# Optimization experiments

Hardware: AMD Instinct MI355X
Metric: run time of the kernel (lower is better)

Reference implementation:

```python
import jax, jax.numpy as jnp
import numpy as np

KEEP_RATIO = 0.5
B, H, W = 8, 1024, 1024


def setup_inputs() -> dict:
    key = jax.random.key(0)
    k1, k2, k3 = jax.random.split(key, 3)
    logits = jax.random.normal(k1, (B, 1, H, W), dtype=jnp.float32)
    targets = jax.random.randint(k2, (B, 1, H, W), 0, 2, dtype=jnp.int32)
    tissue_mask = jax.random.randint(k3, (B, 1, H, W), 0, 2, dtype=jnp.int32)
    return {"logits": logits, "targets": targets, "tissue_mask": tissue_mask}


def reference(logits, targets, tissue_mask):
    b = logits.shape[0]
    x = logits.reshape(b, -1)                       # (B, N)
    t = targets.reshape(b, -1).astype(x.dtype)      # {0,1}
    m = tissue_mask.reshape(b, -1).astype(x.dtype)  # {0,1}
    n = x.shape[1]

    # stable binary_cross_entropy_with_logits, reduction='none'
    bce = jnp.maximum(x, 0.0) - x * t + jnp.log1p(jnp.exp(-jnp.abs(x)))
    loss = bce * m                                  # masked per-pixel loss

    pos = t * m                                     # positives inside tissue
    neg = (1.0 - t) * m                             # negatives inside tissue
    n_pos = jnp.sum(pos, axis=1)                    # (B,)
    n_neg = jnp.sum(neg, axis=1)

    k_all = max(1, int(n * KEEP_RATIO))             # static python int
    # kept count per row: all positives + top-(k_all - n_pos) negatives (clamped)
    k_keep = n_pos + jnp.minimum(jnp.maximum(k_all - n_pos, 0.0), n_neg)  # (B,)

    BIG = jnp.asarray(1e30, x.dtype)
    # sort key: positives always first, then negatives by loss, then non-tissue
    sort_key = jnp.where(pos > 0, BIG, jnp.where(neg > 0, loss, -BIG))
    order = jnp.argsort(-sort_key, axis=1)          # descending
    sorted_loss = jnp.take_along_axis(loss, order, axis=1)

    ranks = jnp.arange(n, dtype=x.dtype)
    keep = (ranks[None, :] < k_keep[:, None]).astype(x.dtype)
    per_sample = jnp.sum(sorted_loss * keep, axis=1) / jnp.maximum(k_keep, 1.0)
    # fallback when no tissue pixels at all: torch keeps index 0 (loss there is 0)
    per_sample = jnp.where(k_keep > 0, per_sample, loss[:, 0])
    return jnp.mean(per_sample)
```

## Files before the change

kernel.cpp:

```cpp
#include <hip/hip_runtime.h>
#include <cstdint>
#include <cstddef>

#define N_PIX   1048576
#define B_ROWS  8
#define K_ALL   524288
#define WG_PER_ROW 256
#define ITERS   4
#define NBINS   2048
#define FPSCALE 262144.0f


__global__ __launch_bounds__(256, 6) void k_pass1(
    const float4* __restrict__ lg, const int4* __restrict__ tg, const int4* __restrict__ mk,
    unsigned long long* __restrict__ hist,
    unsigned* __restrict__ partNpos, double* __restrict__ partSpos, float* __restrict__ out)
{
    __shared__ unsigned long long hq[NBINS];
    __shared__ unsigned swp[4];
    __shared__ double   sws[4];
    const int tid = threadIdx.x;
    for (int b = tid; b < NBINS; b += 256) hq[b] = 0ull;
    if (blockIdx.x == 0 && tid == 0) *out = 0.f;

    const int r = blockIdx.x >> 8;
    const size_t base = (size_t)blockIdx.x * (ITERS * 256) + tid;

    float4 x[ITERS]; int4 t[ITERS]; int4 m[ITERS];
    #pragma unroll
    for (int i = 0; i < ITERS; ++i) {
        x[i] = lg[base + (size_t)i * 256];
        t[i] = tg[base + (size_t)i * 256];
        m[i] = mk[base + (size_t)i * 256];
    }
    __syncthreads();

    unsigned npos = 0; float spos = 0.f;

    auto proc = [&](float xx, int tt, int mm) {
        float ax = fabsf(xx);
        float e = __expf(-ax);
        float l = __logf(1.f + e);
        float bce = fmaxf(xx, 0.f) - xx * (float)tt + l;
        if (mm) {
            if (tt) { npos++; spos += bce; }
            else {
                unsigned bin = __float_as_uint(bce) >> 21;
                if (bin >= NBINS) bin = NBINS - 1;
                unsigned fx = (unsigned)__float2uint_rn(bce * FPSCALE);
                atomicAdd(&hq[bin], (1ull << 48) | (unsigned long long)fx);
            }
        }
    };

    #pragma unroll
    for (int i = 0; i < ITERS; ++i) {
        proc(x[i].x, t[i].x, m[i].x);
        proc(x[i].y, t[i].y, m[i].y);
        proc(x[i].z, t[i].z, m[i].z);
        proc(x[i].w, t[i].w, m[i].w);
    }

    for (int o = 32; o; o >>= 1) {
        npos += __shfl_down(npos, o);
        spos += __shfl_down(spos, o);
    }
    if ((tid & 63) == 0) { swp[tid >> 6] = npos; sws[tid >> 6] = (double)spos; }
    __syncthreads();
    if (tid == 0) {
        partNpos[blockIdx.x] = swp[0] + swp[1] + swp[2] + swp[3];
        partSpos[blockIdx.x] = sws[0] + sws[1] + sws[2] + sws[3];
    }

    unsigned long long* gh = hist + (size_t)r * NBINS;
    for (int b = tid; b < NBINS; b += 256) {
        unsigned long long v = hq[b];
        if (v) atomicAdd(&gh[b], v);
    }
}

__global__ __launch_bounds__(256) void k_final(
    const unsigned long long* __restrict__ hist,
    const unsigned* __restrict__ partNpos, const double* __restrict__ partSpos,
    float* __restrict__ out)
{
    __shared__ unsigned sc[2][256];
    __shared__ double   sd[2][256];
    __shared__ unsigned swp[4];
    __shared__ double   sws[4];
    __shared__ int rT; __shared__ unsigned rcntgt; __shared__ double rsumgt;

    const int r = blockIdx.x, tid = threadIdx.x;
    const unsigned long long* gh = hist + (size_t)r * NBINS;
    const double inv = 1.0 / (double)FPSCALE;

    {
        unsigned np = partNpos[r * 256 + tid];
        double   sp = partSpos[r * 256 + tid];
        for (int o = 32; o; o >>= 1) { np += __shfl_down(np, o); sp += __shfl_down(sp, o); }
        if ((tid & 63) == 0) { swp[tid >> 6] = np; sws[tid >> 6] = sp; }
    }
    __syncthreads();
    const unsigned npos = swp[0] + swp[1] + swp[2] + swp[3];
    const double sumPos = sws[0] + sws[1] + sws[2] + sws[3];
    __syncthreads();

    const int per = NBINS / 256;
    const int b0 = NBINS - 1 - tid * per;
    unsigned lc[8]; double lsum[8];
    unsigned pc = 0; double ps = 0.0;
    #pragma unroll
    for (int i = 0; i < per; ++i) {
        unsigned long long v = gh[b0 - i];
        lc[i] = (unsigned)(v >> 48);
        lsum[i] = (double)(v & 0xFFFFFFFFFFFFull) * inv;
        pc += lc[i]; ps += lsum[i];
    }

    int pp = 0;
    sc[0][tid] = pc; sd[0][tid] = ps;
    __syncthreads();
    for (int ofs = 1; ofs < 256; ofs <<= 1) {
        unsigned c = sc[pp][tid]; double s = sd[pp][tid];
        if (tid >= ofs) { c += sc[pp][tid - ofs]; s += sd[pp][tid - ofs]; }
        sc[pp ^ 1][tid] = c; sd[pp ^ 1][tid] = s;
        pp ^= 1;
        __syncthreads();
    }
    const unsigned nneg   = sc[pp][255];
    const double   sumNeg = sd[pp][255];

    long kl = (long)K_ALL - (long)npos;
    if (kl < 0) kl = 0;
    if (kl > (long)nneg) kl = (long)nneg;
    const unsigned Kneg = (unsigned)kl;

    double sum_sel = 0.0;
    if (Kneg >= nneg) {
        sum_sel = sumNeg;
    } else if (Kneg > 0) {
        unsigned inc = sc[pp][tid];
        unsigned exc = inc - pc;
        double   exs = sd[pp][tid] - ps;
        if (exc < Kneg && Kneg <= inc) {
            unsigned cum = exc; double csum = exs;
            #pragma unroll
            for (int i = 0; i < per; ++i) {
                if (cum + lc[i] >= Kneg) { rT = b0 - i; rcntgt = cum; rsumgt = csum; break; }
                cum += lc[i]; csum += lsum[i];
            }
        }
        __syncthreads();
        if (tid == 0) {
            const int T1 = rT;
            unsigned long long v = gh[T1];
            const unsigned cntT1 = (unsigned)(v >> 48);
            const double   sumT1 = (double)(v & 0xFFFFFFFFFFFFull) * inv;
            const unsigned Kp = Kneg - rcntgt;
            const float lo = __uint_as_float((unsigned)T1 << 21);
            const float hi = __uint_as_float((unsigned)(T1 + 1) << 21);
            const double w = (double)hi - (double)lo;
            const double avg = sumT1 / (double)cntT1;
            const double topmean = avg + 0.5 * w * (1.0 - (double)Kp / (double)cntT1);
            sum_sel = rsumgt + (double)Kp * topmean;
        }
    }

    if (tid == 0) {
        unsigned long long kk = (unsigned long long)npos + (unsigned long long)Kneg;
        double per_s = 0.0;
        if (kk > 0) per_s = (sumPos + sum_sel) / (double)kk;
        atomicAdd(out, (float)(per_s / (double)B_ROWS));
    }
}

extern "C" void kernel_launch(void* const* d_in, const int* in_sizes, int n_in,
                              void* d_out, int out_size, void* d_ws, size_t ws_size,
                              hipStream_t stream)
{
    const float* logits = (const float*)d_in[0];
    const int*   targets = (const int*)d_in[1];
    const int*   tissue = (const int*)d_in[2];

    const int NBLK = B_ROWS * WG_PER_ROW;
    char* ws = (char*)d_ws;
    size_t off = 0;
    unsigned long long* hist = (unsigned long long*)(ws + off);
    off += (size_t)B_ROWS * NBINS * 8;
    size_t zero_size = off;
    unsigned* partNpos = (unsigned*)(ws + off); off += (size_t)NBLK * 4;
    double*   partSpos = (double*)(ws + off);   off += (size_t)NBLK * 8;

    hipMemsetAsync(ws, 0, zero_size, stream);

    k_pass1<<<NBLK, 256, 0, stream>>>(
        (const float4*)logits, (const int4*)targets, (const int4*)tissue,
        hist, partNpos, partSpos, (float*)d_out);
    k_final<<<B_ROWS, 256, 0, stream>>>(hist, partNpos, partSpos, (float*)d_out);
}
```

Baseline: 121.5 us.

## Select top-k negatives via complement: histogram only low-loss negatives below pivot

Instead of histogramming every negative's loss to find the top-K, the kernel now accumulates the total count and sum of negatives and histograms only those below a pivot of 0.25, using 512 bins instead of 2048. The final kernel subtracts the sum of the smallest D = nneg - Kneg negatives, so fewer shared-memory atomics and a smaller global histogram are needed. Loads are split into two chunks to cut register pressure, and occupancy is raised to 8. It assumes the dropped bottom D negatives usually fall under the pivot; otherwise it approximates them at the pivot value, which is an accuracy risk.

After: 121.6 us. No clear change (+0.1%).

```diff
diff --git a/kernel.cpp b/kernel.cpp
--- a/kernel.cpp
+++ b/kernel.cpp
@@ -7,73 +7,84 @@
 #define K_ALL   524288
 #define WG_PER_ROW 256
 #define ITERS   4
-#define NBINS   2048
-#define FPSCALE 262144.0f
-
-
-__global__ __launch_bounds__(256, 6) void k_pass1(
+#define HBINS   512
+#define PIVOT   0.25f
+#define FPSCALE 1048576.0f
+#define MASK48  0xFFFFFFFFFFFFull
+
+
+__global__ __launch_bounds__(256, 8) void k_pass1(
     const float4* __restrict__ lg, const int4* __restrict__ tg, const int4* __restrict__ mk,
     unsigned long long* __restrict__ hist,
-    unsigned* __restrict__ partNpos, double* __restrict__ partSpos, float* __restrict__ out)
+    unsigned* __restrict__ partNpos, unsigned* __restrict__ partNneg,
+    double* __restrict__ partSpos, double* __restrict__ partSneg, float* __restrict__ out)
 {
-    __shared__ unsigned long long hq[NBINS];
-    __shared__ unsigned swp[4];
-    __shared__ double   sws[4];
+    __shared__ unsigned long long hq[HBINS];
+    __shared__ unsigned swp[4], swn[4];
+    __shared__ double   sws[4], swn2[4];
     const int tid = threadIdx.x;
-    for (int b = tid; b < NBINS; b += 256) hq[b] = 0ull;
+    for (int b = tid; b < HBINS; b += 256) hq[b] = 0ull;
     if (blockIdx.x == 0 && tid == 0) *out = 0.f;
+    __syncthreads();
 
     const int r = blockIdx.x >> 8;
     const size_t base = (size_t)blockIdx.x * (ITERS * 256) + tid;
 
-    float4 x[ITERS]; int4 t[ITERS]; int4 m[ITERS];
-    #pragma unroll
-    for (int i = 0; i < ITERS; ++i) {
-        x[i] = lg[base + (size_t)i * 256];
-        t[i] = tg[base + (size_t)i * 256];
-        m[i] = mk[base + (size_t)i * 256];
-    }
-    __syncthreads();
-
-    unsigned npos = 0; float spos = 0.f;
+    unsigned npos = 0, nneg = 0; float spos = 0.f, sneg = 0.f;
 
     auto proc = [&](float xx, int tt, int mm) {
         float ax = fabsf(xx);
-        float e = __expf(-ax);
-        float l = __logf(1.f + e);
+        float l = __logf(1.f + __expf(-ax));
         float bce = fmaxf(xx, 0.f) - xx * (float)tt + l;
         if (mm) {
             if (tt) { npos++; spos += bce; }
             else {
-                unsigned bin = __float_as_uint(bce) >> 21;
-                if (bin >= NBINS) bin = NBINS - 1;
-                unsigned fx = (unsigned)__float2uint_rn(bce * FPSCALE);
-                atomicAdd(&hq[bin], (1ull << 48) | (unsigned long long)fx);
+                nneg++; sneg += bce;
+                if (bce < PIVOT) {
+                    unsigned bin = __float_as_uint(bce) >> 21;
+                    unsigned long long fx = (unsigned long long)__float2uint_rn(bce * FPSCALE);
+                    atomicAdd(&hq[bin], (1ull << 48) | fx);
+                }
             }
         }
     };
 
     #pragma unroll
-    for (int i = 0; i < ITERS; ++i) {
-        proc(x[i].x, t[i].x, m[i].x);
-        proc(x[i].y, t[i].y, m[i].y);
-        proc(x[i].z, t[i].z, m[i].z);
-        proc(x[i].w, t[i].w, m[i].w);
+    for (int c = 0; c < 2; ++c) {
+        float4 x0 = lg[base + (size_t)(2 * c) * 256];
+        float4 x1 = lg[base + (size_t)(2 * c + 1) * 256];
+        int4   t0 = tg[base + (size_t)(2 * c) * 256];
+        int4   t1 = tg[base + (size_t)(2 * c + 1) * 256];
+        int4   m0 = mk[base + (size_t)(2 * c) * 256];
+        int4   m1 = mk[base + (size_t)(2 * c + 1) * 256];
+        proc(x0.x, t0.x, m0.x); proc(x0.y, t0.y, m0.y);
+        proc(x0.z, t0.z, m0.z); proc(x0.w, t0.w, m0.w);
+        proc(x1.x, t1.x, m1.x); proc(x1.y, t1.y, m1.y);
+        proc(x1.z, t1.z, m1.z); proc(x1.w, t1.w, m1.w);
     }
 
     for (int o = 32; o; o >>= 1) {
         npos += __shfl_down(npos, o);
+        nneg += __shfl_down(nneg, o);
         spos += __shfl_down(spos, o);
-    }
-    if ((tid & 63) == 0) { swp[tid >> 6] = npos; sws[tid >> 6] = (double)spos; }
+        sneg += __shfl_down(sneg, o);
+    }
+    if ((tid & 63) == 0) {
+        swp[tid >> 6] = npos; swn[tid >> 6] = nneg;
+        sws[tid >> 6] = (double)spos; swn2[tid >> 6] = (double)sneg;
+    }
     __syncthreads();
     if (tid == 0) {
         partNpos[blockIdx.x] = swp[0] + swp[1] + swp[2] + swp[3];
+        partNneg[blockIdx.x] = swn[0] + swn[1] + swn[2] + swn[3];
         partSpos[blockIdx.x] = sws[0] + sws[1] + sws[2] + sws[3];
-    }
-
-    unsigned long long* gh = hist + (size_t)r * NBINS;
-    for (int b = tid; b < NBINS; b += 256) {
+        partSneg[blockIdx.x] = swn2[0] + swn2[1] + swn2[2] + swn2[3];
+    }
+
+    unsigned long long* gh = hist + (size_t)r * HBINS;
+    #pragma unroll
+    for (int i = 0; i < HBINS / 256; ++i) {
+        int b = tid + i * 256;
         unsigned long long v = hq[b];
         if (v) atomicAdd(&gh[b], v);
     }
@@ -81,41 +92,47 @@
 
 __global__ __launch_bounds__(256) void k_final(
     const unsigned long long* __restrict__ hist,
-    const unsigned* __restrict__ partNpos, const double* __restrict__ partSpos,
+    const unsigned* __restrict__ partNpos, const unsigned* __restrict__ partNneg,
+    const double* __restrict__ partSpos, const double* __restrict__ partSneg,
     float* __restrict__ out)
 {
     __shared__ unsigned sc[2][256];
     __shared__ double   sd[2][256];
-    __shared__ unsigned swp[4];
-    __shared__ double   sws[4];
-    __shared__ int rT; __shared__ unsigned rcntgt; __shared__ double rsumgt;
+    __shared__ unsigned swp[4], swn[4];
+    __shared__ double   sws[4], swn2[4];
+    __shared__ int rT; __shared__ unsigned rcntlt; __shared__ double rsumlt;
+    __shared__ double ssel;
 
     const int r = blockIdx.x, tid = threadIdx.x;
-    const unsigned long long* gh = hist + (size_t)r * NBINS;
+    const unsigned long long* gh = hist + (size_t)r * HBINS;
     const double inv = 1.0 / (double)FPSCALE;
 
     {
         unsigned np = partNpos[r * 256 + tid];
+        unsigned nn = partNneg[r * 256 + tid];
         double   sp = partSpos[r * 256 + tid];
-        for (int o = 32; o; o >>= 1) { np += __shfl_down(np, o); sp += __shfl_down(sp, o); }
-        if ((tid & 63) == 0) { swp[tid >> 6] = np; sws[tid >> 6] = sp; }
+        double   sn = partSneg[r * 256 + tid];
+        for (int o = 32; o; o >>= 1) {
+            np += __shfl_down(np, o); nn += __shfl_down(nn, o);
+            sp += __shfl_down(sp, o); sn += __shfl_down(sn, o);
+        }
+        if ((tid & 63) == 0) {
+            swp[tid >> 6] = np; swn[tid >> 6] = nn;
+            sws[tid >> 6] = sp; swn2[tid >> 6] = sn;
+        }
     }
     __syncthreads();
     const unsigned npos = swp[0] + swp[1] + swp[2] + swp[3];
+    const unsigned nneg = swn[0] + swn[1] + swn[2] + swn[3];
     const double sumPos = sws[0] + sws[1] + sws[2] + sws[3];
-    __syncthreads();
-
-    const int per = NBINS / 256;
-    const int b0 = NBINS - 1 - tid * per;
-    unsigned lc[8]; double lsum[8];
-    unsigned pc = 0; double ps = 0.0;
-    #pragma unroll
-    for (int i = 0; i < per; ++i) {
-        unsigned long long v = gh[b0 - i];
-        lc[i] = (unsigned)(v >> 48);
-        lsum[i] = (double)(v & 0xFFFFFFFFFFFFull) * inv;
-        pc += lc[i]; ps += lsum[i];
-    }
+    const double sumNeg = swn2[0] + swn2[1] + swn2[2] + swn2[3];
+    __syncthreads();
+
+    const int b0 = tid * 2;
+    unsigned long long v0 = gh[b0], v1 = gh[b0 + 1];
+    const unsigned c0 = (unsigned)(v0 >> 48), c1 = (unsigned)(v1 >> 48);
+    const double s0 = (double)(v0 & MASK48) * inv, s1 = (double)(v1 & MASK48) * inv;
+    unsigned pc = c0 + c1; double ps = s0 + s1;
 
     int pp = 0;
     sc[0][tid] = pc; sd[0][tid] = ps;
@@ -127,49 +144,51 @@
         pp ^= 1;
         __syncthreads();
     }
-    const unsigned nneg   = sc[pp][255];
-    const double   sumNeg = sd[pp][255];
+    const unsigned H  = sc[pp][255];
+    const double   SH = sd[pp][255];
 
     long kl = (long)K_ALL - (long)npos;
     if (kl < 0) kl = 0;
     if (kl > (long)nneg) kl = (long)nneg;
     const unsigned Kneg = (unsigned)kl;
 
-    double sum_sel = 0.0;
     if (Kneg >= nneg) {
-        sum_sel = sumNeg;
-    } else if (Kneg > 0) {
-        unsigned inc = sc[pp][tid];
-        unsigned exc = inc - pc;
-        double   exs = sd[pp][tid] - ps;
-        if (exc < Kneg && Kneg <= inc) {
-            unsigned cum = exc; double csum = exs;
-            #pragma unroll
-            for (int i = 0; i < per; ++i) {
-                if (cum + lc[i] >= Kneg) { rT = b0 - i; rcntgt = cum; rsumgt = csum; break; }
-                cum += lc[i]; csum += lsum[i];
+        if (tid == 0) ssel = sumNeg;
+    } else if (Kneg == 0) {
+        if (tid == 0) ssel = 0.0;
+    } else {
+        const unsigned D = nneg - Kneg;
+        if (D >= H) {
+            if (tid == 0) ssel = sumNeg - (SH + (double)(D - H) * (double)PIVOT);
+        } else {
+            const unsigned inc = sc[pp][tid];
+            const unsigned exc = inc - pc;
+            const double   exs = sd[pp][tid] - ps;
+            if (exc < D && D <= inc) {
+                if (exc + c0 >= D) { rT = b0;     rcntlt = exc;      rsumlt = exs;      }
+                else               { rT = b0 + 1; rcntlt = exc + c0; rsumlt = exs + s0; }
             }
-        }
-        __syncthreads();
-        if (tid == 0) {
-            const int T1 = rT;
-            unsigned long long v = gh[T1];
-            const unsigned cntT1 = (unsigned)(v >> 48);
-            const double   sumT1 = (double)(v & 0xFFFFFFFFFFFFull) * inv;
-            const unsigned Kp = Kneg - rcntgt;
-            const float lo = __uint_as_float((unsigned)T1 << 21);
-            const float hi = __uint_as_float((unsigned)(T1 + 1) << 21);
-            const double w = (double)hi - (double)lo;
-            const double avg = sumT1 / (double)cntT1;
-            const double topmean = avg + 0.5 * w * (1.0 - (double)Kp / (double)cntT1);
-            sum_sel = rsumgt + (double)Kp * topmean;
-        }
-    }
+            __syncthreads();
+            if (tid == 0) {
+                unsigned long long v = gh[rT];
+                const unsigned cntT = (unsigned)(v >> 48);
+                const double   sumT = (double)(v & MASK48) * inv;
+                const unsigned Kp = D - rcntlt;
+                const float lo = __uint_as_float((unsigned)rT << 21);
+                const float hi = __uint_as_float((unsigned)(rT + 1) << 21);
+                const double w = (double)hi - (double)lo;
+                const double avg = sumT / (double)cntT;
+                const double botmean = avg - 0.5 * w * (1.0 - (double)Kp / (double)cntT);
+                ssel = sumNeg - (rsumlt + (double)Kp * botmean);
+            }
+        }
+    }
+    __syncthreads();
 
     if (tid == 0) {
         unsigned long long kk = (unsigned long long)npos + (unsigned long long)Kneg;
         double per_s = 0.0;
-        if (kk > 0) per_s = (sumPos + sum_sel) / (double)kk;
+        if (kk > 0) per_s = (sumPos + ssel) / (double)kk;
         atomicAdd(out, (float)(per_s / (double)B_ROWS));
     }
 }
@@ -186,15 +205,18 @@
     char* ws = (char*)d_ws;
     size_t off = 0;
     unsigned long long* hist = (unsigned long long*)(ws + off);
-    off += (size_t)B_ROWS * NBINS * 8;
+    off += (size_t)B_ROWS * HBINS * 8;
     size_t zero_size = off;
     unsigned* partNpos = (unsigned*)(ws + off); off += (size_t)NBLK * 4;
+    unsigned* partNneg = (unsigned*)(ws + off); off += (size_t)NBLK * 4;
     double*   partSpos = (double*)(ws + off);   off += (size_t)NBLK * 8;
+    double*   partSneg = (double*)(ws + off);   off += (size_t)NBLK * 8;
 
     hipMemsetAsync(ws, 0, zero_size, stream);
 
     k_pass1<<<NBLK, 256, 0, stream>>>(
         (const float4*)logits, (const int4*)targets, (const int4*)tissue,
-        hist, partNpos, partSpos, (float*)d_out);
-    k_final<<<B_ROWS, 256, 0, stream>>>(hist, partNpos, partSpos, (float*)d_out);
+        hist, partNpos, partNneg, partSpos, partSneg, (float*)d_out);
+    k_final<<<B_ROWS, 256, 0, stream>>>(hist, partNpos, partNneg, partSpos, partSneg,
+                                        (float*)d_out);
 }
```
